# Kernel optimization log

Hardware: AMD Instinct MI355X
Metric: run time of the kernel (lower is better)

Reference implementation:

```python
import jax, jax.numpy as jnp
import numpy as np

MASK_RATIO = 0.75
LN_EPS = 1e-5

def layer_norm(x, g, b):
    m = jnp.mean(x, axis=-1, keepdims=True)
    v = jnp.mean((x - m) ** 2, axis=-1, keepdims=True)
    return (x - m) * jax.lax.rsqrt(v + LN_EPS) * g + b

def setup_inputs() -> dict:
    key = jax.random.key(0)
    ks = jax.random.split(key, 10)
    B, L, D = 32, 2000, 1024
    s = 0.02
    return {
        "expr": jax.random.normal(ks[0], (B, L), jnp.float32),
        "idx": jax.random.randint(ks[1], (B, L), 0, L),
        "noise": jax.random.uniform(ks[2], (B, L), jnp.float32),
        "pos_table": jax.random.normal(ks[3], (L, D), jnp.float32) * s,
        "cls_token": jax.random.normal(ks[4], (1, 1, D), jnp.float32) * s,
        "w_enc": jax.random.normal(ks[5], (D,), jnp.float32) * s,
        "b_enc": jnp.zeros((D,), jnp.float32),
        "gamma1": jnp.ones((D,), jnp.float32),
        "beta1": jnp.zeros((D,), jnp.float32),
        "W_dec": jax.random.normal(ks[6], (D, D), jnp.float32) * s,
        "b_dec": jnp.zeros((D,), jnp.float32),
        "mask_token": jax.random.normal(ks[7], (D,), jnp.float32) * s,
        "gamma2": jnp.ones((D,), jnp.float32),
        "beta2": jnp.zeros((D,), jnp.float32),
        "W_pred": jax.random.normal(ks[8], (D, 1), jnp.float32) * s,
        "b_pred": jnp.zeros((1,), jnp.float32),
    }

def reference(expr, idx, noise, pos_table, cls_token, w_enc, b_enc, gamma1, beta1,
              W_dec, b_dec, mask_token, gamma2, beta2, W_pred, b_pred):
    B, L = expr.shape
    D = pos_table.shape[1]
    len_keep = int(L * (1.0 - MASK_RATIO))

    # encoder embed: Linear(1 -> D) on expression scalar, plus gene pos embedding
    x = expr[..., None] * w_enc + b_enc + pos_table[idx]          # [B, L, D]

    # random masking (per-sample shuffle by argsort of noise)
    ids_shuffle = jnp.argsort(noise, axis=1)                      # [B, L]
    ids_restore = jnp.argsort(ids_shuffle, axis=1)                # [B, L]
    ids_keep = ids_shuffle[:, :len_keep]
    x_masked = jnp.take_along_axis(x, ids_keep[..., None], axis=1)  # [B, keep, D]
    mask = jnp.concatenate([jnp.zeros((B, len_keep), x.dtype),
                            jnp.ones((B, L - len_keep), x.dtype)], axis=1)
    mask = jnp.take_along_axis(mask, ids_restore, axis=1)         # [B, L]

    # cls token (+ first row of pos table), prepend
    cls = jnp.broadcast_to(cls_token + pos_table[:1][None], (B, 1, D))
    h = jnp.concatenate([cls, x_masked], axis=1)                  # [B, 1+keep, D]
    # NOTE: source Block.forward returns its input unchanged (returns x, not
    # the attention output), so the encoder/decoder block stacks are identities.
    latent = layer_norm(h, gamma1, beta1)                          # [B, 1+keep, D]

    # decoder
    xd = jnp.einsum('bnd,de->bne', latent, W_dec) + b_dec          # [B, 1+keep, D]
    mtok = jnp.broadcast_to(mask_token, (B, L - len_keep, D))
    x_ = jnp.concatenate([xd[:, 1:, :], mtok], axis=1)             # [B, L, D]
    x_ = jnp.take_along_axis(x_, ids_restore[..., None], axis=1)   # unshuffle
    dpos = pos_table[idx]                                          # [B, L, D]
    first = (x_ + dpos)[:, :1, :]  # pos embed only reaches the first token
    xd = jnp.concatenate([first, x_], axis=1)                      # [B, L+1, D]
    xd = layer_norm(xd, gamma2, beta2)
    pred = jnp.einsum('bnd,do->bno', xd, W_pred) + b_pred          # [B, L+1, 1]
    pred = pred[:, 1:, :]                                          # [B, L, 1]

    # masked MSE loss
    target = jnp.nan_to_num(expr)
    loss = jnp.sum((pred[..., 0] - target) ** 2 * mask) / jnp.sum(mask)
    return (loss, pred, mask, latent[:, 0])
```

## Files before the change

kernel.cpp:

```cpp
#include <hip/hip_runtime.h>

typedef __attribute__((ext_vector_type(8))) __bf16 bf16x8;
typedef __attribute__((ext_vector_type(4))) float f32x4;
typedef __attribute__((ext_vector_type(4))) unsigned short us4;

typedef const __attribute__((address_space(1))) void* gas;
typedef __attribute__((address_space(3))) void* las;

static __device__ __forceinline__ unsigned short f2bf(float f) {
  unsigned int u = __float_as_uint(f);
  u += 0x7fffu + ((u >> 16) & 1u);
  return (unsigned short)(u >> 16);
}
static __device__ __forceinline__ float bf2f(unsigned short s) {
  return __uint_as_float(((unsigned int)s) << 16);
}

template <int Q>
__device__ __forceinline__ void btree(float* sm, float* v) {
  const int t = threadIdx.x;
#pragma unroll
  for (int q = 0; q < Q; ++q) sm[q * 256 + t] = v[q];
  __syncthreads();
  for (int o = 128; o > 0; o >>= 1) {
    if (t < o)
#pragma unroll
      for (int q = 0; q < Q; ++q) sm[q * 256 + t] += sm[q * 256 + t + o];
    __syncthreads();
  }
#pragma unroll
  for (int q = 0; q < Q; ++q) v[q] = sm[q * 256];
  __syncthreads();
}

__global__ __launch_bounds__(256) void rank_w(const float* __restrict__ noise,
                                              int* __restrict__ rank,
                                              int* __restrict__ keep) {
  __shared__ alignas(16) float nz[2000];
  __shared__ int pc[256];
  const int b = blockIdx.x;
  const int tile = blockIdx.y;
  const int tid = threadIdx.x;
  const float* nr = noise + b * 2000;
  for (int j = tid; j < 500; j += 256)
    ((float4*)nz)[j] = ((const float4*)nr)[j];
  __syncthreads();
  const int il = tid >> 2;
  const int jq = tid & 3;
  const int i = tile * 64 + il;
  int cnt = 0;
  if (i < 2000) {
    const float ni = nz[i];
    const int j0 = jq * 125;
#pragma unroll 5
    for (int j4 = j0; j4 < j0 + 125; ++j4) {
      float4 v = ((const float4*)nz)[j4];
      const int j = j4 * 4;
      cnt += (int)((v.x < ni) | ((v.x == ni) & (j < i)));
      cnt += (int)((v.y < ni) | ((v.y == ni) & ((j + 1) < i)));
      cnt += (int)((v.z < ni) | ((v.z == ni) & ((j + 2) < i)));
      cnt += (int)((v.w < ni) | ((v.w == ni) & ((j + 3) < i)));
    }
  }
  pc[tid] = cnt;
  __syncthreads();
  if (jq == 0 && i < 2000) {
    const int total = pc[tid] + pc[tid + 1] + pc[tid + 2] + pc[tid + 3];
    rank[b * 2000 + i] = total;
    if (total < 500) keep[b * 500 + total] = i;
  }
}

__global__ __launch_bounds__(256) void trans_w(const float* __restrict__ W,
                                               unsigned short* __restrict__ Bt) {
  __shared__ float tile[32][33];
  const int tx = threadIdx.x & 31, ty = threadIdx.x >> 5;
  const int r0 = blockIdx.y * 32, c0 = blockIdx.x * 32;
#pragma unroll
  for (int k = 0; k < 4; ++k)
    tile[ty + k * 8][tx] = W[(size_t)(r0 + ty + k * 8) * 1024 + c0 + tx];
  __syncthreads();
#pragma unroll
  for (int k = 0; k < 4; ++k) {
    const int cr = ty + k * 8;
    Bt[(size_t)(c0 + cr) * 1024 + r0 + tx] = f2bf(tile[tx][cr]);
  }
}

__global__ __launch_bounds__(256) void pre_w(const float* __restrict__ mtok,
                                             const float* __restrict__ g2,
                                             const float* __restrict__ be2,
                                             const float* __restrict__ Wp,
                                             const float* __restrict__ bp,
                                             float* __restrict__ scal) {
  __shared__ float sm[512];
  const int t = threadIdx.x;
  float4 x = ((const float4*)mtok)[t];
  float v[2];
  v[0] = x.x + x.y + x.z + x.w;
  v[1] = x.x * x.x + x.y * x.y + x.z * x.z + x.w * x.w;
  btree<2>(sm, v);
  const float mean = v[0] * (1.f / 1024.f);
  const float r = rsqrtf(v[1] * (1.f / 1024.f) - mean * mean + 1e-5f);
  float4 g = ((const float4*)g2)[t];
  float4 be = ((const float4*)be2)[t];
  float4 w = ((const float4*)Wp)[t];
  float d[1];
  d[0] = ((x.x - mean) * r * g.x + be.x) * w.x +
         ((x.y - mean) * r * g.y + be.y) * w.y +
         ((x.z - mean) * r * g.z + be.z) * w.z +
         ((x.w - mean) * r * g.w + be.w) * w.w;
  btree<1>(sm, d);
  if (t == 0) scal[0] = d[0] + bp[0];
}

__global__ __launch_bounds__(256) void enc_w(
    const float* __restrict__ expr, const int* __restrict__ idx,
    const float* __restrict__ pos, const float* __restrict__ cls,
    const float* __restrict__ wenc, const float* __restrict__ benc,
    const float* __restrict__ g1, const float* __restrict__ be1,
    const int* __restrict__ keep, unsigned short* __restrict__ latent,
    float* __restrict__ out_l0) {
  __shared__ float sm[512];
  const int bx = blockIdx.x;
  const int b = bx / 501, n = bx % 501;
  const int t = threadIdx.x;
  float4 x;
  int m = 0;
  if (n == 0) {
    float4 c = ((const float4*)cls)[t];
    float4 p = ((const float4*)pos)[t];
    x.x = c.x + p.x; x.y = c.y + p.y; x.z = c.z + p.z; x.w = c.w + p.w;
  } else {
    m = b * 500 + n - 1;
    const int i = keep[m];
    const float e = expr[b * 2000 + i];
    const int row = idx[b * 2000 + i];
    float4 w = ((const float4*)wenc)[t];
    float4 bb = ((const float4*)benc)[t];
    float4 p = ((const float4*)(pos + (size_t)row * 1024))[t];
    x.x = fmaf(e, w.x, bb.x) + p.x;
    x.y = fmaf(e, w.y, bb.y) + p.y;
    x.z = fmaf(e, w.z, bb.z) + p.z;
    x.w = fmaf(e, w.w, bb.w) + p.w;
  }
  float v[2];
  v[0] = x.x + x.y + x.z + x.w;
  v[1] = x.x * x.x + x.y * x.y + x.z * x.z + x.w * x.w;
  btree<2>(sm, v);
  const float mean = v[0] * (1.f / 1024.f);
  const float r = rsqrtf(v[1] * (1.f / 1024.f) - mean * mean + 1e-5f);
  float4 g = ((const float4*)g1)[t];
  float4 be = ((const float4*)be1)[t];
  const float y0 = (x.x - mean) * r * g.x + be.x;
  const float y1 = (x.y - mean) * r * g.y + be.y;
  const float y2 = (x.z - mean) * r * g.z + be.z;
  const float y3 = (x.w - mean) * r * g.w + be.w;
  if (n == 0) {
    float* o = out_l0 + b * 1024 + t * 4;
    o[0] = y0; o[1] = y1; o[2] = y2; o[3] = y3;
  } else {
    us4 o; o.x = f2bf(y0); o.y = f2bf(y1); o.z = f2bf(y2); o.w = f2bf(y3);
    ((us4*)(latent + (size_t)m * 1024))[t] = o;
  }
}

__global__ __launch_bounds__(256, 3) void gemm_w(
    const unsigned short* __restrict__ A,
    const unsigned short* __restrict__ Bt,
    const float* __restrict__ bdec,
    unsigned short* __restrict__ Xd) {
  __shared__ alignas(16) char lds[16384];
  const int tid = threadIdx.x;
  const int wid = tid >> 6;
  const int lane = tid & 63;
  const int bm = blockIdx.x;
  const int bn = blockIdx.y;
  const int wm = wid >> 1, wn = wid & 1;

  const int srow = tid >> 2;
  const int g = (tid & 3) ^ ((tid >> 3) & 3);
  const unsigned short* aS = A + (size_t)(bm * 128 + srow) * 1024 + g * 8;
  const unsigned short* bS = Bt + (size_t)(bn * 128 + srow) * 1024 + g * 8;
  char* ldsA = lds;
  char* ldsB = lds + 8192;
  char* stA = ldsA + wid * 1024;
  char* stB = ldsB + wid * 1024;

  f32x4 acc[4][4];
#pragma unroll
  for (int i = 0; i < 4; ++i)
#pragma unroll
    for (int j = 0; j < 4; ++j) { f32x4 z = {0.f, 0.f, 0.f, 0.f}; acc[i][j] = z; }

  const int r = lane & 15;
  const int gg = lane >> 4;
  const int swz = ((gg ^ ((r >> 1) & 3)) * 16);
  const int aRd = (wm * 64 + r) * 64 + swz;
  const int bRd = (wn * 64 + r) * 64 + swz;

  for (int ks = 0; ks < 1024; ks += 32) {
    __builtin_amdgcn_global_load_lds((gas)(aS + ks), (las)(stA), 16, 0, 0);
    __builtin_amdgcn_global_load_lds((gas)(aS + 64 * 1024 + ks), (las)(stA + 4096), 16, 0, 0);
    __builtin_amdgcn_global_load_lds((gas)(bS + ks), (las)(stB), 16, 0, 0);
    __builtin_amdgcn_global_load_lds((gas)(bS + 64 * 1024 + ks), (las)(stB + 4096), 16, 0, 0);
    __syncthreads();
    bf16x8 af[4], bfr[4];
#pragma unroll
    for (int mf = 0; mf < 4; ++mf) af[mf] = *(const bf16x8*)(ldsA + aRd + mf * 1024);
#pragma unroll
    for (int nf = 0; nf < 4; ++nf) bfr[nf] = *(const bf16x8*)(ldsB + bRd + nf * 1024);
#pragma unroll
    for (int mf = 0; mf < 4; ++mf)
#pragma unroll
      for (int nf = 0; nf < 4; ++nf)
        acc[mf][nf] = __builtin_amdgcn_mfma_f32_16x16x32_bf16(af[mf], bfr[nf], acc[mf][nf], 0, 0, 0);
    __syncthreads();
  }
  const int dr = lane >> 4, dc = lane & 15;
#pragma unroll
  for (int nf = 0; nf < 4; ++nf) {
    const int col = bn * 128 + wn * 64 + nf * 16 + dc;
    const float bias = bdec[col];
#pragma unroll
    for (int mf = 0; mf < 4; ++mf) {
      const size_t rbase = (size_t)(bm * 128 + wm * 64 + mf * 16 + dr * 4) * 1024 + col;
      f32x4 v = acc[mf][nf];
#pragma unroll
      for (int q = 0; q < 4; ++q) Xd[rbase + (size_t)q * 1024] = f2bf(v[q] + bias);
    }
  }
}

__global__ __launch_bounds__(256) void pred_w(
    const unsigned short* __restrict__ Xd, const float* __restrict__ g2,
    const float* __restrict__ be2, const float* __restrict__ Wp,
    const float* __restrict__ bp, const int* __restrict__ keep,
    float* __restrict__ out_pred) {
  __shared__ float sm[512];
  const int m = blockIdx.x;
  const int b = m / 500;
  const int t = threadIdx.x;
  us4 xu = ((const us4*)(Xd + (size_t)m * 1024))[t];
  const float x0 = bf2f(xu.x), x1 = bf2f(xu.y), x2 = bf2f(xu.z), x3 = bf2f(xu.w);
  float v[2];
  v[0] = x0 + x1 + x2 + x3;
  v[1] = x0 * x0 + x1 * x1 + x2 * x2 + x3 * x3;
  btree<2>(sm, v);
  const float mean = v[0] * (1.f / 1024.f);
  const float r = rsqrtf(v[1] * (1.f / 1024.f) - mean * mean + 1e-5f);
  float4 g = ((const float4*)g2)[t];
  float4 be = ((const float4*)be2)[t];
  float4 w = ((const float4*)Wp)[t];
  float d[1];
  d[0] = ((x0 - mean) * r * g.x + be.x) * w.x +
         ((x1 - mean) * r * g.y + be.y) * w.y +
         ((x2 - mean) * r * g.z + be.z) * w.z +
         ((x3 - mean) * r * g.w + be.w) * w.w;
  btree<1>(sm, d);
  if (t == 0) {
    const int i = keep[m];
    out_pred[b * 2000 + i] = d[0] + bp[0];
  }
}

__global__ __launch_bounds__(256) void mask_w(
    const int* __restrict__ rank, const float* __restrict__ expr,
    const float* __restrict__ scal, float* __restrict__ out_mask,
    float* __restrict__ out_pred, float* __restrict__ partial) {
  __shared__ float sm[256];
  const int t = blockIdx.x * 256 + threadIdx.x;
  const float pm = scal[0];
  const bool msk = rank[t] >= 500;
  out_mask[t] = msk ? 1.0f : 0.0f;
  float c[1] = {0.f};
  if (msk) {
    out_pred[t] = pm;
    float tv = expr[t];
    if (isnan(tv)) tv = 0.f;
    const float d = pm - tv;
    c[0] = d * d;
  }
  btree<1>(sm, c);
  if (threadIdx.x == 0) partial[blockIdx.x] = c[0];
}

__global__ __launch_bounds__(256) void fin_w(const float* __restrict__ partial,
                                             float* __restrict__ out) {
  __shared__ float sm[256];
  const int t = threadIdx.x;
  float v[1];
  v[0] = (t < 250) ? partial[t] : 0.f;
  btree<1>(sm, v);
  if (t == 0) out[0] = v[0] * (1.f / 48000.f);
}

extern "C" void kernel_launch(void* const* d_in, const int* in_sizes, int n_in,
                              void* d_out, int out_size, void* d_ws, size_t ws_size,
                              hipStream_t stream) {
  const float* expr = (const float*)d_in[0];
  const int* idx = (const int*)d_in[1];
  const float* noise = (const float*)d_in[2];
  const float* pos = (const float*)d_in[3];
  const float* cls = (const float*)d_in[4];
  const float* wenc = (const float*)d_in[5];
  const float* benc = (const float*)d_in[6];
  const float* g1 = (const float*)d_in[7];
  const float* be1 = (const float*)d_in[8];
  const float* Wdec = (const float*)d_in[9];
  const float* bdec = (const float*)d_in[10];
  const float* mtok = (const float*)d_in[11];
  const float* g2 = (const float*)d_in[12];
  const float* be2 = (const float*)d_in[13];
  const float* Wp = (const float*)d_in[14];
  const float* bp = (const float*)d_in[15];
  float* out = (float*)d_out;

  char* ws = (char*)d_ws;
  int* rank = (int*)ws;
  int* keep = (int*)(ws + 256000);
  float* scal = (float*)(ws + 320000);
  float* partial = (float*)(ws + 320064);
  unsigned short* Bt = (unsigned short*)(ws + 321536);
  unsigned short* latent = (unsigned short*)(ws + 321536 + 2097152);
  unsigned short* Xd = (unsigned short*)(ws + 321536 + 2097152 + 32768000);
  if (ws_size < (size_t)(321536 + 2097152 + 2 * 32768000)) return;

  float* out_pred = out + 1;
  float* out_mask = out + 64001;
  float* out_l0 = out + 128001;

  rank_w<<<dim3(32, 32), 256, 0, stream>>>(noise, rank, keep);
  trans_w<<<dim3(32, 32), 256, 0, stream>>>(Wdec, Bt);
  pre_w<<<1, 256, 0, stream>>>(mtok, g2, be2, Wp, bp, scal);
  enc_w<<<32 * 501, 256, 0, stream>>>(expr, idx, pos, cls, wenc, benc, g1, be1,
                                      keep, latent, out_l0);
  gemm_w<<<dim3(125, 8), 256, 0, stream>>>(latent, Bt, bdec, Xd);
  pred_w<<<16000, 256, 0, stream>>>(Xd, g2, be2, Wp, bp, keep, out_pred);
  mask_w<<<250, 256, 0, stream>>>(rank, expr, scal, out_mask, out_pred, partial);
  fin_w<<<1, 256, 0, stream>>>(partial, out);
}
```

Measured before the change: 218.7 us.

## Fuse decoder LayerNorm and prediction projection into GEMM epilogue via row-sum atomics

The GEMM epilogue no longer writes the bf16 decoder activations. Each row instead reduces sum, sum of squares and the gamma·W_pred-weighted sum across lanes, and adds them to a small per-row buffer with atomics. The separate pred_w kernel is removed. The mask kernel rebuilds the prediction algebraically from these three sums and from constants precomputed in pre_w. This drops a 32MB write and re-read of the intermediate, at the cost of atomic contention across the 8 N-blocks, a memset, and the single-pass variance formula in fp32.

```diff
diff --git a/kernel.cpp b/kernel.cpp
--- a/kernel.cpp
+++ b/kernel.cpp
@@ -92,8 +92,9 @@
                                              const float* __restrict__ be2,
                                              const float* __restrict__ Wp,
                                              const float* __restrict__ bp,
-                                             float* __restrict__ scal) {
-  __shared__ float sm[512];
+                                             float* __restrict__ scal,
+                                             float* __restrict__ uw) {
+  __shared__ float sm[768];
   const int t = threadIdx.x;
   float4 x = ((const float4*)mtok)[t];
   float v[2];
@@ -105,13 +106,22 @@
   float4 g = ((const float4*)g2)[t];
   float4 be = ((const float4*)be2)[t];
   float4 w = ((const float4*)Wp)[t];
-  float d[1];
+  float4 u;
+  u.x = g.x * w.x; u.y = g.y * w.y; u.z = g.z * w.z; u.w = g.w * w.w;
+  ((float4*)uw)[t] = u;
+  float d[3];
   d[0] = ((x.x - mean) * r * g.x + be.x) * w.x +
          ((x.y - mean) * r * g.y + be.y) * w.y +
          ((x.z - mean) * r * g.z + be.z) * w.z +
          ((x.w - mean) * r * g.w + be.w) * w.w;
-  btree<1>(sm, d);
-  if (t == 0) scal[0] = d[0] + bp[0];
+  d[1] = u.x + u.y + u.z + u.w;
+  d[2] = be.x * w.x + be.y * w.y + be.z * w.z + be.w * w.w;
+  btree<3>(sm, d);
+  if (t == 0) {
+    scal[0] = d[0] + bp[0];
+    scal[1] = d[1];
+    scal[2] = d[2] + bp[0];
+  }
 }
 
 __global__ __launch_bounds__(256) void enc_w(
@@ -168,8 +178,8 @@
 __global__ __launch_bounds__(256, 3) void gemm_w(
     const unsigned short* __restrict__ A,
     const unsigned short* __restrict__ Bt,
-    const float* __restrict__ bdec,
-    unsigned short* __restrict__ Xd) {
+    const float* __restrict__ bdec, const float* __restrict__ uw,
+    float* __restrict__ sums) {
   __shared__ alignas(16) char lds[16384];
   const int tid = threadIdx.x;
   const int wid = tid >> 6;
@@ -217,61 +227,50 @@
         acc[mf][nf] = __builtin_amdgcn_mfma_f32_16x16x32_bf16(af[mf], bfr[nf], acc[mf][nf], 0, 0, 0);
     __syncthreads();
   }
-  const int dr = lane >> 4, dc = lane & 15;
+  const int dc = r, dr = gg;
+  float biasv[4], uv[4];
 #pragma unroll
   for (int nf = 0; nf < 4; ++nf) {
     const int col = bn * 128 + wn * 64 + nf * 16 + dc;
-    const float bias = bdec[col];
-#pragma unroll
-    for (int mf = 0; mf < 4; ++mf) {
-      const size_t rbase = (size_t)(bm * 128 + wm * 64 + mf * 16 + dr * 4) * 1024 + col;
-      f32x4 v = acc[mf][nf];
-#pragma unroll
-      for (int q = 0; q < 4; ++q) Xd[rbase + (size_t)q * 1024] = f2bf(v[q] + bias);
+    biasv[nf] = bdec[col];
+    uv[nf] = uw[col];
+  }
+#pragma unroll
+  for (int mf = 0; mf < 4; ++mf) {
+#pragma unroll
+    for (int q = 0; q < 4; ++q) {
+      float s = 0.f, s2 = 0.f, su = 0.f;
+#pragma unroll
+      for (int nf = 0; nf < 4; ++nf) {
+        const float x = acc[mf][nf][q] + biasv[nf];
+        s += x; s2 += x * x; su += uv[nf] * x;
+      }
+#pragma unroll
+      for (int msk = 1; msk < 16; msk <<= 1) {
+        s += __shfl_xor(s, msk, 64);
+        s2 += __shfl_xor(s2, msk, 64);
+        su += __shfl_xor(su, msk, 64);
+      }
+      if (dc == 0) {
+        const int row = bm * 128 + wm * 64 + mf * 16 + dr * 4 + q;
+        atomicAdd(&sums[row * 3 + 0], s);
+        atomicAdd(&sums[row * 3 + 1], s2);
+        atomicAdd(&sums[row * 3 + 2], su);
+      }
     }
-  }
-}
-
-__global__ __launch_bounds__(256) void pred_w(
-    const unsigned short* __restrict__ Xd, const float* __restrict__ g2,
-    const float* __restrict__ be2, const float* __restrict__ Wp,
-    const float* __restrict__ bp, const int* __restrict__ keep,
-    float* __restrict__ out_pred) {
-  __shared__ float sm[512];
-  const int m = blockIdx.x;
-  const int b = m / 500;
-  const int t = threadIdx.x;
-  us4 xu = ((const us4*)(Xd + (size_t)m * 1024))[t];
-  const float x0 = bf2f(xu.x), x1 = bf2f(xu.y), x2 = bf2f(xu.z), x3 = bf2f(xu.w);
-  float v[2];
-  v[0] = x0 + x1 + x2 + x3;
-  v[1] = x0 * x0 + x1 * x1 + x2 * x2 + x3 * x3;
-  btree<2>(sm, v);
-  const float mean = v[0] * (1.f / 1024.f);
-  const float r = rsqrtf(v[1] * (1.f / 1024.f) - mean * mean + 1e-5f);
-  float4 g = ((const float4*)g2)[t];
-  float4 be = ((const float4*)be2)[t];
-  float4 w = ((const float4*)Wp)[t];
-  float d[1];
-  d[0] = ((x0 - mean) * r * g.x + be.x) * w.x +
-         ((x1 - mean) * r * g.y + be.y) * w.y +
-         ((x2 - mean) * r * g.z + be.z) * w.z +
-         ((x3 - mean) * r * g.w + be.w) * w.w;
-  btree<1>(sm, d);
-  if (t == 0) {
-    const int i = keep[m];
-    out_pred[b * 2000 + i] = d[0] + bp[0];
   }
 }
 
 __global__ __launch_bounds__(256) void mask_w(
     const int* __restrict__ rank, const float* __restrict__ expr,
-    const float* __restrict__ scal, float* __restrict__ out_mask,
-    float* __restrict__ out_pred, float* __restrict__ partial) {
+    const float* __restrict__ scal, const float* __restrict__ sums,
+    float* __restrict__ out_mask, float* __restrict__ out_pred,
+    float* __restrict__ partial) {
   __shared__ float sm[256];
   const int t = blockIdx.x * 256 + threadIdx.x;
   const float pm = scal[0];
-  const bool msk = rank[t] >= 500;
+  const int rk = rank[t];
+  const bool msk = rk >= 500;
   out_mask[t] = msk ? 1.0f : 0.0f;
   float c[1] = {0.f};
   if (msk) {
@@ -280,6 +279,14 @@
     if (isnan(tv)) tv = 0.f;
     const float d = pm - tv;
     c[0] = d * d;
+  } else {
+    const int m = (t / 2000) * 500 + rk;
+    const float s = sums[m * 3 + 0];
+    const float s2 = sums[m * 3 + 1];
+    const float su = sums[m * 3 + 2];
+    const float mean = s * (1.f / 1024.f);
+    const float rr = rsqrtf(s2 * (1.f / 1024.f) - mean * mean + 1e-5f);
+    out_pred[t] = rr * (su - mean * scal[1]) + scal[2];
   }
   btree<1>(sm, c);
   if (threadIdx.x == 0) partial[blockIdx.x] = c[0];
@@ -321,22 +328,24 @@
   int* keep = (int*)(ws + 256000);
   float* scal = (float*)(ws + 320000);
   float* partial = (float*)(ws + 320064);
-  unsigned short* Bt = (unsigned short*)(ws + 321536);
-  unsigned short* latent = (unsigned short*)(ws + 321536 + 2097152);
-  unsigned short* Xd = (unsigned short*)(ws + 321536 + 2097152 + 32768000);
-  if (ws_size < (size_t)(321536 + 2097152 + 2 * 32768000)) return;
+  float* uw = (float*)(ws + 321088);
+  unsigned short* Bt = (unsigned short*)(ws + 325184);
+  unsigned short* latent = (unsigned short*)(ws + 325184 + 2097152);
+  float* sums = (float*)(ws + 325184 + 2097152 + 32768000);
+  if (ws_size < (size_t)(325184 + 2097152 + 32768000 + 192000)) return;
 
   float* out_pred = out + 1;
   float* out_mask = out + 64001;
   float* out_l0 = out + 128001;
 
+  hipMemsetAsync(sums, 0, 16000 * 3 * sizeof(float), stream);
   rank_w<<<dim3(32, 32), 256, 0, stream>>>(noise, rank, keep);
   trans_w<<<dim3(32, 32), 256, 0, stream>>>(Wdec, Bt);
-  pre_w<<<1, 256, 0, stream>>>(mtok, g2, be2, Wp, bp, scal);
+  pre_w<<<1, 256, 0, stream>>>(mtok, g2, be2, Wp, bp, scal, uw);
   enc_w<<<32 * 501, 256, 0, stream>>>(expr, idx, pos, cls, wenc, benc, g1, be1,
                                       keep, latent, out_l0);
-  gemm_w<<<dim3(125, 8), 256, 0, stream>>>(latent, Bt, bdec, Xd);
-  pred_w<<<16000, 256, 0, stream>>>(Xd, g2, be2, Wp, bp, keep, out_pred);
-  mask_w<<<250, 256, 0, stream>>>(rank, expr, scal, out_mask, out_pred, partial);
+  gemm_w<<<dim3(125, 8), 256, 0, stream>>>(latent, Bt, bdec, uw, sums);
+  mask_w<<<250, 256, 0, stream>>>(rank, expr, scal, sums, out_mask, out_pred,
+                                  partial);
   fin_w<<<1, 256, 0, stream>>>(partial, out);
 }
```

Result: slower. 224.6 us (+2.7%).
